# Optimization experiments

Measured on AMD Instinct MI355X. Metric: run time of the kernel, lower is better.

## Reference

```python
import jax, jax.numpy as jnp
import numpy as np

N, E, R = 50000, 1600000, 8
IN_F, HID_F, OUT_F = 128, 64, 64


def setup_inputs() -> dict:
    key = jax.random.key(0)
    ks = jax.random.split(key, 9)
    x = jax.random.normal(ks[0], (N, IN_F), dtype=jnp.float32)
    edge_index = jax.random.randint(ks[1], (2, E), 0, N, dtype=jnp.int64)
    edge_type = jax.random.randint(ks[2], (E,), 0, R, dtype=jnp.int64)
    # layer 1 params (scaled like glorot)
    s1 = 1.0 / np.sqrt(IN_F)
    W1_rel = jax.random.normal(ks[3], (R, IN_F, HID_F), dtype=jnp.float32) * s1
    W1_root = jax.random.normal(ks[4], (IN_F, HID_F), dtype=jnp.float32) * s1
    b1 = jnp.zeros((HID_F,), dtype=jnp.float32)
    # layer 2 params
    s2 = 1.0 / np.sqrt(HID_F)
    W2_rel = jax.random.normal(ks[5], (R, HID_F, OUT_F), dtype=jnp.float32) * s2
    W2_root = jax.random.normal(ks[6], (HID_F, OUT_F), dtype=jnp.float32) * s2
    b2 = jnp.zeros((OUT_F,), dtype=jnp.float32)
    return {"x": x, "edge_index": edge_index, "edge_type": edge_type,
            "W1_rel": W1_rel, "W1_root": W1_root, "b1": b1,
            "W2_rel": W2_rel, "W2_root": W2_root, "b2": b2}


def _rgcn_conv(x, src, dst, etype, W_rel, W_root, b):
    """PyG RGCNConv: root transform + per-relation mean-aggregated messages."""
    n = x.shape[0]
    r = W_rel.shape[0]
    # per-relation transform of all node features: [R, N, H]
    xw = jnp.einsum('nd,rdh->rnh', x, W_rel)
    # per-edge message: transformed source feature under the edge's relation
    msg = xw[etype, src]  # [E, H]
    # mean normalization per (dst, relation) pair
    key = dst * r + etype  # [E]
    cnt = jax.ops.segment_sum(jnp.ones(etype.shape, dtype=x.dtype), key,
                              num_segments=n * r)
    inv = 1.0 / jnp.maximum(cnt, 1.0)
    msg = msg * inv[key][:, None]
    # scatter-add into target nodes
    agg = jax.ops.segment_sum(msg, dst, num_segments=n)  # [N, H]
    return agg + x @ W_root + b


def reference(x, edge_index, edge_type, W1_rel, W1_root, b1, W2_rel, W2_root, b2):
    src, dst = edge_index[0], edge_index[1]
    h = _rgcn_conv(x, src, dst, edge_type, W1_rel, W1_root, b1)
    h = jax.nn.relu(h)
    out = _rgcn_conv(h, src, dst, edge_type, W2_rel, W2_root, b2)
    return out
```

## Files before the change

kernel.cpp:

```cpp
#include <hip/hip_runtime.h>


constexpr int NN  = 50000;
constexpr int NE  = 1600000;
constexpr int NR  = 8;
constexpr int FIN = 128;
constexpr int FH  = 64;

constexpr int BSH = 7;
constexpr int BN  = 1 << BSH;
constexpr int NB  = (NN + BN - 1) >> BSH;
constexpr int CAP = 6144;
constexpr int CH  = 4096;
constexpr int NAPP = (NE + CH - 1) / CH;
constexpr unsigned XWMAX = (unsigned)(NN - 1) * (NR * 64) + (NR - 1) * 64;

typedef __attribute__((ext_vector_type(8))) short bf16x8;
typedef __attribute__((ext_vector_type(4))) float f32x4;

__device__ __forceinline__ unsigned short f2bf(float f) {
  unsigned u = __float_as_uint(f);
  u = (u + 0x7fff + ((u >> 16) & 1)) >> 16;
  return (unsigned short)u;
}
__device__ __forceinline__ float bf2f(unsigned short b) {
  return __uint_as_float(((unsigned)b) << 16);
}
__device__ __forceinline__ bool edge_ok(unsigned s, unsigned d, unsigned r) {
  return s < NN && d < NN && r < NR;
}

__device__ void append_body(char* smem, int bx,
                            const int* __restrict__ src,
                            const int* __restrict__ dst,
                            const int* __restrict__ et,
                            int* __restrict__ bcur,
                            unsigned* __restrict__ brecs) {
  uint2* stage = (uint2*)smem;
  int* h     = (int*)(smem + (size_t)CH * 8);
  int* gbase = h + NB;
  int* sbase = gbase + NB;
  int* scur  = sbase + NB;
  int* wtot  = scur + NB;

  const int t  = threadIdx.x;
  const int c0 = bx * CH;
  const int m  = min(CH, NE - c0);

  for (int i = t; i < NB; i += 256) h[i] = 0;
  __syncthreads();

  for (int i = t; i < m; i += 256) {
    const unsigned s = (unsigned)src[c0 + i];
    const unsigned d = (unsigned)dst[c0 + i];
    const unsigned r = (unsigned)et[c0 + i];
    if (edge_ok(s, d, r)) atomicAdd(&h[d >> BSH], 1);
  }
  __syncthreads();

  const int v0 = (2 * t < NB) ? h[2 * t] : 0;
  const int v1 = (2 * t + 1 < NB) ? h[2 * t + 1] : 0;
  if (2 * t < NB     && v0) gbase[2 * t]     = atomicAdd(&bcur[2 * t], v0);
  if (2 * t + 1 < NB && v1) gbase[2 * t + 1] = atomicAdd(&bcur[2 * t + 1], v1);
  const int s = v0 + v1;
  int incl = s;
#pragma unroll
  for (int o = 1; o < 64; o <<= 1) {
    int u = __shfl_up(incl, o, 64);
    if ((t & 63) >= o) incl += u;
  }
  if ((t & 63) == 63) wtot[t >> 6] = incl;
  __syncthreads();
  int wo = 0;
  for (int w = 0; w < (t >> 6); ++w) wo += wtot[w];
  const int e = wo + incl - s;
  if (2 * t < NB)     { sbase[2 * t] = e;          scur[2 * t] = e; }
  if (2 * t + 1 < NB) { sbase[2 * t + 1] = e + v0; scur[2 * t + 1] = e + v0; }
  __syncthreads();

  for (int i = t; i < m; i += 256) {
    const unsigned sv = (unsigned)src[c0 + i];
    const unsigned d  = (unsigned)dst[c0 + i];
    const unsigned r  = (unsigned)et[c0 + i];
    if (edge_ok(sv, d, r)) {
      const int p = atomicAdd(&scur[d >> BSH], 1);
      if (p < CH) stage[p] = make_uint2((sv << 10) | (((unsigned)d & (BN - 1)) << 3) | r, d);
    }
  }
  __syncthreads();

  const int M = min(sbase[NB - 1] + h[NB - 1], CH);
  for (int j = t; j < M; j += 256) {
    const uint2 rec = stage[j];
    const int b = (int)(rec.y >> BSH);
    const int idx = min(gbase[b] + (j - sbase[b]), NB * CAP - 1);
    brecs[idx] = rec.x;
  }
}

__global__ void __launch_bounds__(256) bucket_finalize(
    const int* __restrict__ bcur, const unsigned* __restrict__ brecs,
    int* __restrict__ row_start, int* __restrict__ deg,
    unsigned* __restrict__ recs) {
  const int b    = blockIdx.x;
  const int base = b * CAP;
  const int m    = min(bcur[b] - base, CAP);
  const int d0   = b << BSH;
  __shared__ int cnt[BN * NR];
  __shared__ int curs[BN * NR];
  __shared__ int wtot[4];
  const int t = threadIdx.x;

  for (int i = t; i < BN * NR; i += 256) cnt[i] = 0;
  __syncthreads();
  for (int i = t; i < m; i += 256) {
    const unsigned rec = brecs[base + i];
    const int dl = (int)((rec >> 3) & (BN - 1));
    const int r  = (int)(rec & 7);
    atomicAdd(&cnt[dl * NR + r], 1);
  }
  __syncthreads();

  const int c0 = cnt[t * 4], c1 = cnt[t * 4 + 1], c2 = cnt[t * 4 + 2], c3 = cnt[t * 4 + 3];
  const int s = c0 + c1 + c2 + c3;
  int incl = s;
#pragma unroll
  for (int o = 1; o < 64; o <<= 1) {
    int u = __shfl_up(incl, o, 64);
    if ((t & 63) >= o) incl += u;
  }
  if ((t & 63) == 63) wtot[t >> 6] = incl;
  __syncthreads();
  int wo = 0;
  for (int w = 0; w < (t >> 6); ++w) wo += wtot[w];
  const int e = wo + incl - s;
  curs[t * 4]     = e;
  curs[t * 4 + 1] = e + c0;
  curs[t * 4 + 2] = e + c0 + c1;
  curs[t * 4 + 3] = e + c0 + c1 + c2;
  __syncthreads();

  if (t < BN) {
    const int d = d0 + t;
    if (d < NN) {
      const int start = curs[t * NR];
      const int end   = (t == BN - 1) ? m : curs[(t + 1) * NR];
      row_start[d] = base + start;
      deg[d]       = end - start;
    }
  }
  __syncthreads();

  for (int i = t; i < m; i += 256) {
    const unsigned rec = brecs[base + i];
    const int dl = (int)((rec >> 3) & (BN - 1));
    const int r  = (int)(rec & 7);
    const unsigned sv = rec >> 10;
    const int p  = atomicAdd(&curs[dl * NR + r], 1);
    const unsigned cn = (unsigned)min(cnt[dl * NR + r], 127);
    recs[base + min(p, CAP - 1)] = (cn << 25) | (sv << 9) | ((unsigned)r << 6);
  }
}

__global__ void prep(const float* __restrict__ W1r, const float* __restrict__ W1o,
                     const float* __restrict__ W2r, const float* __restrict__ W2o,
                     unsigned short* __restrict__ Wt1,
                     unsigned short* __restrict__ Wt2,
                     int* __restrict__ bcur) {
  const int i  = blockIdx.x * blockDim.x + threadIdx.x;
  if (i < NB) bcur[i] = i * CAP;
  const int n1 = (NR + 1) * 64 * FIN;
  const int n2 = (NR + 1) * 64 * FH;
  if (i < n1) {
    const int g = i / (64 * FIN), rem = i % (64 * FIN);
    const int n = rem / FIN, k = rem % FIN;
    const float* W = (g < NR) ? (W1r + (size_t)g * FIN * 64) : W1o;
    Wt1[i] = f2bf(W[k * 64 + n]);
  } else if (i < n1 + n2) {
    const int j = i - n1;
    const int g = j / (64 * FH), rem = j % (64 * FH);
    const int n = rem / FH, k = rem % FH;
    const float* W = (g < NR) ? (W2r + (size_t)g * FH * 64) : W2o;
    Wt2[j] = f2bf(W[k * 64 + n]);
  }
}

template <int K, bool A_FP32>
__device__ void gemm_body(char* smem, int bx,
                          const void* __restrict__ Av,
                          const unsigned short* __restrict__ Wt,
                          const float* __restrict__ bias,
                          unsigned short* __restrict__ xw,
                          float* __restrict__ root_out) {
  constexpr int KP  = K + 8;
  constexpr int NCH = 64 * (K / 8) / 256;
  constexpr int NKC = K / 32;
  unsigned short* Bs0 = (unsigned short*)smem;
  const int n0  = bx * 64;
  const int tid = threadIdx.x;
  const int wave = tid >> 6, lane = tid & 63;
  const int i16 = lane & 15, quad = lane >> 4;
  const int r0 = wave * 16 + i16;
  const int arow = n0 + r0;

  bf16x8 afrag[NKC];
  if constexpr (A_FP32) {
    const float* A = (const float*)Av;
#pragma unroll
    for (int kc = 0; kc < NKC; ++kc) {
      bf16x8 v = {};
      if (arow < NN) {
        const float* p = A + (size_t)arow * K + kc * 32 + quad * 8;
        const float4 f0 = *(const float4*)p;
        const float4 f1 = *(const float4*)(p + 4);
        v[0] = f2bf(f0.x); v[1] = f2bf(f0.y); v[2] = f2bf(f0.z); v[3] = f2bf(f0.w);
        v[4] = f2bf(f1.x); v[5] = f2bf(f1.y); v[6] = f2bf(f1.z); v[7] = f2bf(f1.w);
      }
      afrag[kc] = v;
    }
  } else {
    const unsigned short* A = (const unsigned short*)Av;
#pragma unroll
    for (int kc = 0; kc < NKC; ++kc) {
      bf16x8 v = {};
      if (arow < NN) v = *(const bf16x8*)(A + (size_t)arow * K + kc * 32 + quad * 8);
      afrag[kc] = v;
    }
  }

  for (int c = 0; c < NCH; ++c) {
    const int idx = tid + c * 256;
    const int row = idx / (K / 8), kp = (idx % (K / 8)) * 8;
    *(bf16x8*)(Bs0 + row * KP + kp) = *(const bf16x8*)(Wt + idx * 8);
  }
  __syncthreads();

  for (int g = 0; g <= NR; ++g) {
    const int buf = g & 1;
    unsigned short* Bc = Bs0 + buf * 64 * KP;
    unsigned short* Bn = Bs0 + (buf ^ 1) * 64 * KP;
    bf16x8 breg[NCH];
    if (g < NR) {
      const unsigned short* Wn = Wt + (size_t)(g + 1) * 64 * K;
#pragma unroll
      for (int c = 0; c < NCH; ++c) breg[c] = *(const bf16x8*)(Wn + (tid + c * 256) * 8);
    }

    f32x4 acc[4] = {};
#pragma unroll
    for (int kc = 0; kc < NKC; ++kc) {
      const int k0 = kc * 32 + quad * 8;
      const bf16x8 a0 = afrag[kc];
      const bf16x8 b0 = *(const bf16x8*)(Bc + (i16)      * KP + k0);
      const bf16x8 b1 = *(const bf16x8*)(Bc + (i16 + 16) * KP + k0);
      const bf16x8 b2 = *(const bf16x8*)(Bc + (i16 + 32) * KP + k0);
      const bf16x8 b3 = *(const bf16x8*)(Bc + (i16 + 48) * KP + k0);
      acc[0] = __builtin_amdgcn_mfma_f32_16x16x32_bf16(a0, b0, acc[0], 0, 0, 0);
      acc[1] = __builtin_amdgcn_mfma_f32_16x16x32_bf16(a0, b1, acc[1], 0, 0, 0);
      acc[2] = __builtin_amdgcn_mfma_f32_16x16x32_bf16(a0, b2, acc[2], 0, 0, 0);
      acc[3] = __builtin_amdgcn_mfma_f32_16x16x32_bf16(a0, b3, acc[3], 0, 0, 0);
    }

    if (g < NR) {
#pragma unroll
      for (int c = 0; c < NCH; ++c) {
        const int idx = tid + c * 256;
        const int row = idx / (K / 8), kp = (idx % (K / 8)) * 8;
        *(bf16x8*)(Bn + row * KP + kp) = breg[c];
      }
#pragma unroll
      for (int reg = 0; reg < 4; ++reg) {
        const int n = n0 + wave * 16 + quad * 4 + reg;
        if (n >= NN) continue;
        unsigned short* p = xw + (size_t)n * (NR * 64) + g * 64 + i16;
#pragma unroll
        for (int ct = 0; ct < 4; ++ct) p[ct * 16] = f2bf(acc[ct][reg]);
      }
    } else {
      float bv[4];
#pragma unroll
      for (int ct = 0; ct < 4; ++ct) bv[ct] = bias[ct * 16 + i16];
#pragma unroll
      for (int reg = 0; reg < 4; ++reg) {
        const int n = n0 + wave * 16 + quad * 4 + reg;
        if (n >= NN) continue;
        float* p = root_out + (size_t)n * 64 + i16;
#pragma unroll
        for (int ct = 0; ct < 4; ++ct) p[ct * 16] = acc[ct][reg] + bv[ct];
      }
    }
    __syncthreads();
  }
}

__global__ void __launch_bounds__(256) fused_append_gemm1(
    const int* __restrict__ src, const int* __restrict__ dst,
    const int* __restrict__ et, int* __restrict__ bcur,
    unsigned* __restrict__ brecs,
    const float* __restrict__ A, const unsigned short* __restrict__ Wt,
    const float* __restrict__ bias, unsigned short* __restrict__ xw,
    float* __restrict__ root_out) {
  extern __shared__ char smem[];
  const int bx = (int)blockIdx.x;
  if (bx % 3 == 2 && bx / 3 < NAPP)
    append_body(smem, bx / 3, src, dst, et, bcur, brecs);
  else
    gemm_body<FIN, true>(smem, bx - (bx + 1) / 3, A, Wt, bias, xw, root_out);
}

__global__ void __launch_bounds__(256) gemm_l2(
    const unsigned short* __restrict__ A, const unsigned short* __restrict__ Wt,
    const float* __restrict__ bias, unsigned short* __restrict__ xw,
    float* __restrict__ out) {
  extern __shared__ char smem[];
  gemm_body<FH, false>(smem, (int)blockIdx.x, A, Wt, bias, xw, out);
}

template <bool RELU_BF16>
__global__ void __launch_bounds__(256) agg_csr(
    const int* __restrict__ row_start, const int* __restrict__ deg,
    const unsigned* __restrict__ recs, const unsigned short* __restrict__ xw,
    const float* __restrict__ root,
    float* __restrict__ out_f32, unsigned short* __restrict__ out_b16) {
  const int gid  = blockIdx.x * blockDim.x + threadIdx.x;
  const int lane = gid & 63;
  const int d    = gid >> 6;
  if (d >= NN) return;
  const int e  = lane >> 3;
  const int l8 = lane & 7;
  const int base = row_start[d];
  const int n    = deg[d];
  const unsigned* po = recs + base;
  const unsigned short* xp = xw + l8 * 8;
  float a[8] = {};

  int i0 = 0;
  for (; i0 + 32 < n; i0 += 64) {
    unsigned rr[8];
#pragma unroll
    for (int sl = 0; sl < 8; ++sl) {
      const int i = i0 + e + 8 * sl;
      rr[sl] = (i < n) ? po[i] : 0u;
    }
    bf16x8 vv[8];
#pragma unroll
    for (int sl = 0; sl < 8; ++sl) {
      const unsigned u = min(rr[sl] & 0x01FFFFFFu, XWMAX);
      vv[sl] = *(const bf16x8*)(xp + u);
    }
#pragma unroll
    for (int sl = 0; sl < 8; ++sl) {
      float w = __builtin_amdgcn_rcpf((float)(rr[sl] >> 25));
      if (i0 + e + 8 * sl >= n) w = 0.f;
#pragma unroll
      for (int q = 0; q < 8; ++q) a[q] += bf2f((unsigned short)vv[sl][q]) * w;
    }
  }
  if (i0 < n) {
    const int i = i0 + e;
    const unsigned r0 = (i      < n) ? po[i]      : 0u;
    const unsigned r1 = (i + 8  < n) ? po[i + 8]  : 0u;
    const unsigned r2 = (i + 16 < n) ? po[i + 16] : 0u;
    const unsigned r3 = (i + 24 < n) ? po[i + 24] : 0u;
    const unsigned u0 = min(r0 & 0x01FFFFFFu, XWMAX);
    const unsigned u1 = min(r1 & 0x01FFFFFFu, XWMAX);
    const unsigned u2 = min(r2 & 0x01FFFFFFu, XWMAX);
    const unsigned u3 = min(r3 & 0x01FFFFFFu, XWMAX);
    const bf16x8 v0 = *(const bf16x8*)(xp + u0);
    const bf16x8 v1 = *(const bf16x8*)(xp + u1);
    const bf16x8 v2 = *(const bf16x8*)(xp + u2);
    const bf16x8 v3 = *(const bf16x8*)(xp + u3);
    float w0 = __builtin_amdgcn_rcpf((float)(r0 >> 25));
    float w1 = __builtin_amdgcn_rcpf((float)(r1 >> 25));
    float w2 = __builtin_amdgcn_rcpf((float)(r2 >> 25));
    float w3 = __builtin_amdgcn_rcpf((float)(r3 >> 25));
    if (i      >= n) w0 = 0.f;
    if (i + 8  >= n) w1 = 0.f;
    if (i + 16 >= n) w2 = 0.f;
    if (i + 24 >= n) w3 = 0.f;
#pragma unroll
    for (int q = 0; q < 8; ++q) a[q] += bf2f((unsigned short)v0[q]) * w0;
#pragma unroll
    for (int q = 0; q < 8; ++q) a[q] += bf2f((unsigned short)v1[q]) * w1;
#pragma unroll
    for (int q = 0; q < 8; ++q) a[q] += bf2f((unsigned short)v2[q]) * w2;
#pragma unroll
    for (int q = 0; q < 8; ++q) a[q] += bf2f((unsigned short)v3[q]) * w3;
  }

#pragma unroll
  for (int q = 0; q < 8; ++q) {
    a[q] += __shfl_xor(a[q], 8, 64);
    a[q] += __shfl_xor(a[q], 16, 64);
    a[q] += __shfl_xor(a[q], 32, 64);
  }

  if (e == 0) {
    const float4 r0 = *(const float4*)(root + (size_t)d * 64 + l8 * 8);
    const float4 r1 = *(const float4*)(root + (size_t)d * 64 + l8 * 8 + 4);
    const float o[8] = {r0.x + a[0], r0.y + a[1], r0.z + a[2], r0.w + a[3],
                        r1.x + a[4], r1.y + a[5], r1.z + a[6], r1.w + a[7]};
    if (RELU_BF16) {
      bf16x8 ov;
#pragma unroll
      for (int q = 0; q < 8; ++q) ov[q] = (short)f2bf(fmaxf(o[q], 0.f));
      *(bf16x8*)(out_b16 + (size_t)d * 64 + l8 * 8) = ov;
    } else {
      *(float4*)(out_f32 + (size_t)d * 64 + l8 * 8)     = make_float4(o[0], o[1], o[2], o[3]);
      *(float4*)(out_f32 + (size_t)d * 64 + l8 * 8 + 4) = make_float4(o[4], o[5], o[6], o[7]);
    }
  }
}

extern "C" void kernel_launch(void* const* d_in, const int* in_sizes, int n_in,
                              void* d_out, int out_size, void* d_ws, size_t ws_size,
                              hipStream_t stream) {
  const float* x   = (const float*)d_in[0];
  const int*   ei  = (const int*)d_in[1];
  const int*   et  = (const int*)d_in[2];
  const float* W1r = (const float*)d_in[3];
  const float* W1o = (const float*)d_in[4];
  const float* b1  = (const float*)d_in[5];
  const float* W2r = (const float*)d_in[6];
  const float* W2o = (const float*)d_in[7];
  const float* b2  = (const float*)d_in[8];
  float* out = (float*)d_out;

  const int* src = ei;
  const int* dst = ei + NE;

  char* ws = (char*)d_ws;
  size_t off = 0;
  auto alloc = [&](size_t bytes) {
    void* p = ws + off; off += (bytes + 255) & ~(size_t)255; return p;
  };
  int*   bcur      = (int*)alloc((size_t)NB * 4);
  int*   row_start = (int*)alloc((size_t)NN * 4);
  int*   deg       = (int*)alloc((size_t)NN * 4);
  unsigned* brecs  = (unsigned*)alloc((size_t)NB * CAP * 4);
  unsigned* offs   = (unsigned*)alloc((size_t)NB * CAP * 4);
  unsigned short* xw    = (unsigned short*)alloc((size_t)NN * NR * 64 * 2);
  unsigned short* hb    = (unsigned short*)alloc((size_t)NN * FH * 2);
  float*          hroot = (float*)alloc((size_t)NN * 64 * 4);
  unsigned short* Wt1   = (unsigned short*)alloc((size_t)(NR + 1) * 64 * FIN * 2);
  unsigned short* Wt2   = (unsigned short*)alloc((size_t)(NR + 1) * 64 * FH * 2);

  const int nprep = (NR + 1) * 64 * (FIN + FH);
  prep<<<(nprep + 255) / 256, 256, 0, stream>>>(W1r, W1o, W2r, W2o, Wt1, Wt2, bcur);

  const int gemm_blocks = (NN + 63) / 64;
  const int agg_blocks  = (NN * 64 + 255) / 256;
  constexpr int SM1 = CH * 8 + 4 * NB * 4 + 16;
  constexpr int SM2 = 2 * 64 * (FH + 8) * 2;

  fused_append_gemm1<<<NAPP + gemm_blocks, 256, SM1, stream>>>(
      src, dst, et, bcur, brecs, x, Wt1, b1, xw, hroot);
  bucket_finalize<<<NB, 256, 0, stream>>>(bcur, brecs, row_start, deg, offs);

  agg_csr<true><<<agg_blocks, 256, 0, stream>>>(row_start, deg, offs, xw, hroot, nullptr, hb);
  gemm_l2<<<gemm_blocks, 256, SM2, stream>>>(hb, Wt2, b2, xw, out);
  agg_csr<false><<<agg_blocks, 256, 0, stream>>>(row_start, deg, offs, xw, out, out, nullptr);
}
```

Baseline: 239.4 us.

## Split fused append/GEMM1 kernel, vectorize GEMM stores, store layer-1 root in bf16

The fused kernel that interleaved edge-bucket append blocks with layer-1 GEMM blocks is split into two separate launches, so each can use its own shared-memory size and occupancy. The MFMA operand order is swapped so each lane holds four consecutive output columns, which turns scalar bf16/fp32 stores into 8-byte and 16-byte vector stores. The layer-1 root output is stored as bf16 instead of fp32 to halve that traffic. The aggregation kernel also predicates the upper gather slots and tail loads to skip out-of-range reads. The split loses the overlap between the append and GEMM phases and adds a launch, and the bf16 root adds rounding error.

```diff
diff --git a/kernel.cpp b/kernel.cpp
--- a/kernel.cpp
+++ b/kernel.cpp
@@ -16,6 +16,7 @@
 constexpr unsigned XWMAX = (unsigned)(NN - 1) * (NR * 64) + (NR - 1) * 64;
 
 typedef __attribute__((ext_vector_type(8))) short bf16x8;
+typedef __attribute__((ext_vector_type(4))) short bf16x4;
 typedef __attribute__((ext_vector_type(4))) float f32x4;
 
 __device__ __forceinline__ unsigned short f2bf(float f) {
@@ -30,21 +31,15 @@
   return s < NN && d < NN && r < NR;
 }
 
-__device__ void append_body(char* smem, int bx,
-                            const int* __restrict__ src,
-                            const int* __restrict__ dst,
-                            const int* __restrict__ et,
-                            int* __restrict__ bcur,
-                            unsigned* __restrict__ brecs) {
-  uint2* stage = (uint2*)smem;
-  int* h     = (int*)(smem + (size_t)CH * 8);
-  int* gbase = h + NB;
-  int* sbase = gbase + NB;
-  int* scur  = sbase + NB;
-  int* wtot  = scur + NB;
-
+__global__ void __launch_bounds__(256) bucket_append(
+    const int* __restrict__ src, const int* __restrict__ dst,
+    const int* __restrict__ et, int* __restrict__ bcur,
+    unsigned* __restrict__ brecs) {
+  __shared__ uint2 stage[CH];
+  __shared__ int h[NB], gbase[NB], sbase[NB], scur[NB];
+  __shared__ int wtot[4];
   const int t  = threadIdx.x;
-  const int c0 = bx * CH;
+  const int c0 = blockIdx.x * CH;
   const int m  = min(CH, NE - c0);
 
   for (int i = t; i < NB; i += 256) h[i] = 0;
@@ -185,13 +180,13 @@
   }
 }
 
-template <int K, bool A_FP32>
+template <int K, bool A_FP32, bool ROOT_BF16>
 __device__ void gemm_body(char* smem, int bx,
                           const void* __restrict__ Av,
                           const unsigned short* __restrict__ Wt,
                           const float* __restrict__ bias,
                           unsigned short* __restrict__ xw,
-                          float* __restrict__ root_out) {
+                          void* __restrict__ root_out) {
   constexpr int KP  = K + 8;
   constexpr int NCH = 64 * (K / 8) / 256;
   constexpr int NKC = K / 32;
@@ -200,8 +195,7 @@
   const int tid = threadIdx.x;
   const int wave = tid >> 6, lane = tid & 63;
   const int i16 = lane & 15, quad = lane >> 4;
-  const int r0 = wave * 16 + i16;
-  const int arow = n0 + r0;
+  const int node = n0 + wave * 16 + i16;
 
   bf16x8 afrag[NKC];
   if constexpr (A_FP32) {
@@ -209,8 +203,8 @@
 #pragma unroll
     for (int kc = 0; kc < NKC; ++kc) {
       bf16x8 v = {};
-      if (arow < NN) {
-        const float* p = A + (size_t)arow * K + kc * 32 + quad * 8;
+      if (node < NN) {
+        const float* p = A + (size_t)node * K + kc * 32 + quad * 8;
         const float4 f0 = *(const float4*)p;
         const float4 f1 = *(const float4*)(p + 4);
         v[0] = f2bf(f0.x); v[1] = f2bf(f0.y); v[2] = f2bf(f0.z); v[3] = f2bf(f0.w);
@@ -223,7 +217,7 @@
 #pragma unroll
     for (int kc = 0; kc < NKC; ++kc) {
       bf16x8 v = {};
-      if (arow < NN) v = *(const bf16x8*)(A + (size_t)arow * K + kc * 32 + quad * 8);
+      if (node < NN) v = *(const bf16x8*)(A + (size_t)node * K + kc * 32 + quad * 8);
       afrag[kc] = v;
     }
   }
@@ -255,10 +249,10 @@
       const bf16x8 b1 = *(const bf16x8*)(Bc + (i16 + 16) * KP + k0);
       const bf16x8 b2 = *(const bf16x8*)(Bc + (i16 + 32) * KP + k0);
       const bf16x8 b3 = *(const bf16x8*)(Bc + (i16 + 48) * KP + k0);
-      acc[0] = __builtin_amdgcn_mfma_f32_16x16x32_bf16(a0, b0, acc[0], 0, 0, 0);
-      acc[1] = __builtin_amdgcn_mfma_f32_16x16x32_bf16(a0, b1, acc[1], 0, 0, 0);
-      acc[2] = __builtin_amdgcn_mfma_f32_16x16x32_bf16(a0, b2, acc[2], 0, 0, 0);
-      acc[3] = __builtin_amdgcn_mfma_f32_16x16x32_bf16(a0, b3, acc[3], 0, 0, 0);
+      acc[0] = __builtin_amdgcn_mfma_f32_16x16x32_bf16(b0, a0, acc[0], 0, 0, 0);
+      acc[1] = __builtin_amdgcn_mfma_f32_16x16x32_bf16(b1, a0, acc[1], 0, 0, 0);
+      acc[2] = __builtin_amdgcn_mfma_f32_16x16x32_bf16(b2, a0, acc[2], 0, 0, 0);
+      acc[3] = __builtin_amdgcn_mfma_f32_16x16x32_bf16(b3, a0, acc[3], 0, 0, 0);
     }
 
     if (g < NR) {
@@ -268,44 +262,44 @@
         const int row = idx / (K / 8), kp = (idx % (K / 8)) * 8;
         *(bf16x8*)(Bn + row * KP + kp) = breg[c];
       }
-#pragma unroll
-      for (int reg = 0; reg < 4; ++reg) {
-        const int n = n0 + wave * 16 + quad * 4 + reg;
-        if (n >= NN) continue;
-        unsigned short* p = xw + (size_t)n * (NR * 64) + g * 64 + i16;
-#pragma unroll
-        for (int ct = 0; ct < 4; ++ct) p[ct * 16] = f2bf(acc[ct][reg]);
-      }
-    } else {
-      float bv[4];
-#pragma unroll
-      for (int ct = 0; ct < 4; ++ct) bv[ct] = bias[ct * 16 + i16];
-#pragma unroll
-      for (int reg = 0; reg < 4; ++reg) {
-        const int n = n0 + wave * 16 + quad * 4 + reg;
-        if (n >= NN) continue;
-        float* p = root_out + (size_t)n * 64 + i16;
-#pragma unroll
-        for (int ct = 0; ct < 4; ++ct) p[ct * 16] = acc[ct][reg] + bv[ct];
+      if (node < NN) {
+        unsigned short* p = xw + (size_t)node * (NR * 64) + g * 64 + quad * 4;
+#pragma unroll
+        for (int ct = 0; ct < 4; ++ct) {
+          bf16x4 ov;
+          ov[0] = (short)f2bf(acc[ct][0]); ov[1] = (short)f2bf(acc[ct][1]);
+          ov[2] = (short)f2bf(acc[ct][2]); ov[3] = (short)f2bf(acc[ct][3]);
+          *(bf16x4*)(p + ct * 16) = ov;
+        }
+      }
+    } else if (node < NN) {
+#pragma unroll
+      for (int ct = 0; ct < 4; ++ct) {
+        const float4 bv = *(const float4*)(bias + ct * 16 + quad * 4);
+        const float o0 = acc[ct][0] + bv.x, o1 = acc[ct][1] + bv.y;
+        const float o2 = acc[ct][2] + bv.z, o3 = acc[ct][3] + bv.w;
+        if constexpr (ROOT_BF16) {
+          unsigned short* p = (unsigned short*)root_out + (size_t)node * 64 + ct * 16 + quad * 4;
+          bf16x4 ov;
+          ov[0] = (short)f2bf(o0); ov[1] = (short)f2bf(o1);
+          ov[2] = (short)f2bf(o2); ov[3] = (short)f2bf(o3);
+          *(bf16x4*)p = ov;
+        } else {
+          float* p = (float*)root_out + (size_t)node * 64 + ct * 16 + quad * 4;
+          *(float4*)p = make_float4(o0, o1, o2, o3);
+        }
       }
     }
     __syncthreads();
   }
 }
 
-__global__ void __launch_bounds__(256) fused_append_gemm1(
-    const int* __restrict__ src, const int* __restrict__ dst,
-    const int* __restrict__ et, int* __restrict__ bcur,
-    unsigned* __restrict__ brecs,
+__global__ void __launch_bounds__(256) gemm_l1(
     const float* __restrict__ A, const unsigned short* __restrict__ Wt,
     const float* __restrict__ bias, unsigned short* __restrict__ xw,
-    float* __restrict__ root_out) {
+    unsigned short* __restrict__ hroot) {
   extern __shared__ char smem[];
-  const int bx = (int)blockIdx.x;
-  if (bx % 3 == 2 && bx / 3 < NAPP)
-    append_body(smem, bx / 3, src, dst, et, bcur, brecs);
-  else
-    gemm_body<FIN, true>(smem, bx - (bx + 1) / 3, A, Wt, bias, xw, root_out);
+  gemm_body<FIN, true, true>(smem, (int)blockIdx.x, A, Wt, bias, xw, hroot);
 }
 
 __global__ void __launch_bounds__(256) gemm_l2(
@@ -313,14 +307,14 @@
     const float* __restrict__ bias, unsigned short* __restrict__ xw,
     float* __restrict__ out) {
   extern __shared__ char smem[];
-  gemm_body<FH, false>(smem, (int)blockIdx.x, A, Wt, bias, xw, out);
+  gemm_body<FH, false, false>(smem, (int)blockIdx.x, A, Wt, bias, xw, out);
 }
 
 template <bool RELU_BF16>
 __global__ void __launch_bounds__(256) agg_csr(
     const int* __restrict__ row_start, const int* __restrict__ deg,
     const unsigned* __restrict__ recs, const unsigned short* __restrict__ xw,
-    const float* __restrict__ root,
+    const void* __restrict__ rootv,
     float* __restrict__ out_f32, unsigned short* __restrict__ out_b16) {
   const int gid  = blockIdx.x * blockDim.x + threadIdx.x;
   const int lane = gid & 63;
@@ -344,9 +338,18 @@
     }
     bf16x8 vv[8];
 #pragma unroll
-    for (int sl = 0; sl < 8; ++sl) {
+    for (int sl = 0; sl < 4; ++sl) {
       const unsigned u = min(rr[sl] & 0x01FFFFFFu, XWMAX);
       vv[sl] = *(const bf16x8*)(xp + u);
+    }
+#pragma unroll
+    for (int sl = 4; sl < 8; ++sl) {
+      bf16x8 v = {};
+      if (i0 + e + 8 * sl < n) {
+        const unsigned u = min(rr[sl] & 0x01FFFFFFu, XWMAX);
+        v = *(const bf16x8*)(xp + u);
+      }
+      vv[sl] = v;
     }
 #pragma unroll
     for (int sl = 0; sl < 8; ++sl) {
@@ -357,35 +360,29 @@
     }
   }
   if (i0 < n) {
-    const int i = i0 + e;
-    const unsigned r0 = (i      < n) ? po[i]      : 0u;
-    const unsigned r1 = (i + 8  < n) ? po[i + 8]  : 0u;
-    const unsigned r2 = (i + 16 < n) ? po[i + 16] : 0u;
-    const unsigned r3 = (i + 24 < n) ? po[i + 24] : 0u;
-    const unsigned u0 = min(r0 & 0x01FFFFFFu, XWMAX);
-    const unsigned u1 = min(r1 & 0x01FFFFFFu, XWMAX);
-    const unsigned u2 = min(r2 & 0x01FFFFFFu, XWMAX);
-    const unsigned u3 = min(r3 & 0x01FFFFFFu, XWMAX);
-    const bf16x8 v0 = *(const bf16x8*)(xp + u0);
-    const bf16x8 v1 = *(const bf16x8*)(xp + u1);
-    const bf16x8 v2 = *(const bf16x8*)(xp + u2);
-    const bf16x8 v3 = *(const bf16x8*)(xp + u3);
-    float w0 = __builtin_amdgcn_rcpf((float)(r0 >> 25));
-    float w1 = __builtin_amdgcn_rcpf((float)(r1 >> 25));
-    float w2 = __builtin_amdgcn_rcpf((float)(r2 >> 25));
-    float w3 = __builtin_amdgcn_rcpf((float)(r3 >> 25));
-    if (i      >= n) w0 = 0.f;
-    if (i + 8  >= n) w1 = 0.f;
-    if (i + 16 >= n) w2 = 0.f;
-    if (i + 24 >= n) w3 = 0.f;
-#pragma unroll
-    for (int q = 0; q < 8; ++q) a[q] += bf2f((unsigned short)v0[q]) * w0;
-#pragma unroll
-    for (int q = 0; q < 8; ++q) a[q] += bf2f((unsigned short)v1[q]) * w1;
-#pragma unroll
-    for (int q = 0; q < 8; ++q) a[q] += bf2f((unsigned short)v2[q]) * w2;
-#pragma unroll
-    for (int q = 0; q < 8; ++q) a[q] += bf2f((unsigned short)v3[q]) * w3;
+    unsigned rr[4];
+    bf16x8 vv[4];
+#pragma unroll
+    for (int sl = 0; sl < 4; ++sl) {
+      const int i = i0 + e + 8 * sl;
+      rr[sl] = (i < n) ? po[i] : 0u;
+    }
+#pragma unroll
+    for (int sl = 0; sl < 4; ++sl) {
+      bf16x8 v = {};
+      if (i0 + e + 8 * sl < n) {
+        const unsigned u = min(rr[sl] & 0x01FFFFFFu, XWMAX);
+        v = *(const bf16x8*)(xp + u);
+      }
+      vv[sl] = v;
+    }
+#pragma unroll
+    for (int sl = 0; sl < 4; ++sl) {
+      float w = __builtin_amdgcn_rcpf((float)(rr[sl] >> 25));
+      if (i0 + e + 8 * sl >= n) w = 0.f;
+#pragma unroll
+      for (int q = 0; q < 8; ++q) a[q] += bf2f((unsigned short)vv[sl][q]) * w;
+    }
   }
 
 #pragma unroll
@@ -396,10 +393,20 @@
   }
 
   if (e == 0) {
-    const float4 r0 = *(const float4*)(root + (size_t)d * 64 + l8 * 8);
-    const float4 r1 = *(const float4*)(root + (size_t)d * 64 + l8 * 8 + 4);
-    const float o[8] = {r0.x + a[0], r0.y + a[1], r0.z + a[2], r0.w + a[3],
-                        r1.x + a[4], r1.y + a[5], r1.z + a[6], r1.w + a[7]};
+    float r[8];
+    if constexpr (RELU_BF16) {
+      const bf16x8 rv = *(const bf16x8*)((const unsigned short*)rootv + (size_t)d * 64 + l8 * 8);
+#pragma unroll
+      for (int q = 0; q < 8; ++q) r[q] = bf2f((unsigned short)rv[q]);
+    } else {
+      const float4 r0 = *(const float4*)((const float*)rootv + (size_t)d * 64 + l8 * 8);
+      const float4 r1 = *(const float4*)((const float*)rootv + (size_t)d * 64 + l8 * 8 + 4);
+      r[0] = r0.x; r[1] = r0.y; r[2] = r0.z; r[3] = r0.w;
+      r[4] = r1.x; r[5] = r1.y; r[6] = r1.z; r[7] = r1.w;
+    }
+    float o[8];
+#pragma unroll
+    for (int q = 0; q < 8; ++q) o[q] = r[q] + a[q];
     if (RELU_BF16) {
       bf16x8 ov;
 #pragma unroll
@@ -441,7 +448,7 @@
   unsigned* offs   = (unsigned*)alloc((size_t)NB * CAP * 4);
   unsigned short* xw    = (unsigned short*)alloc((size_t)NN * NR * 64 * 2);
   unsigned short* hb    = (unsigned short*)alloc((size_t)NN * FH * 2);
-  float*          hroot = (float*)alloc((size_t)NN * 64 * 4);
+  unsigned short* hroot = (unsigned short*)alloc((size_t)NN * 64 * 2);
   unsigned short* Wt1   = (unsigned short*)alloc((size_t)(NR + 1) * 64 * FIN * 2);
   unsigned short* Wt2   = (unsigned short*)alloc((size_t)(NR + 1) * 64 * FH * 2);
 
@@ -450,13 +457,13 @@
 
   const int gemm_blocks = (NN + 63) / 64;
   const int agg_blocks  = (NN * 64 + 255) / 256;
-  constexpr int SM1 = CH * 8 + 4 * NB * 4 + 16;
+  constexpr int SM1 = 2 * 64 * (FIN + 8) * 2;
   constexpr int SM2 = 2 * 64 * (FH + 8) * 2;
 
-  fused_append_gemm1<<<NAPP + gemm_blocks, 256, SM1, stream>>>(
-      src, dst, et, bcur, brecs, x, Wt1, b1, xw, hroot);
+  bucket_append<<<NAPP, 256, 0, stream>>>(src, dst, et, bcur, brecs);
   bucket_finalize<<<NB, 256, 0, stream>>>(bcur, brecs, row_start, deg, offs);
 
+  gemm_l1<<<gemm_blocks, 256, SM1, stream>>>(x, Wt1, b1, xw, hroot);
   agg_csr<true><<<agg_blocks, 256, 0, stream>>>(row_start, deg, offs, xw, hroot, nullptr, hb);
   gemm_l2<<<gemm_blocks, 256, SM2, stream>>>(hb, Wt2, b2, xw, out);
   agg_csr<false><<<agg_blocks, 256, 0, stream>>>(row_start, deg, offs, xw, out, out, nullptr);
```

Measured after the change: 265.3 us. 10.8% more time.
